# Performance work log

Hardware: AMD Instinct MI355X
Metric: run time of the kernel (lower is better)

Reference implementation:

```python
import jax, jax.numpy as jnp
import numpy as np

EMBED_DIM = 1024
NUM_HEADS = 16
HEAD_DIM = EMBED_DIM // NUM_HEADS
EPS = 1e-6


def setup_inputs() -> dict:
    key = jax.random.key(0)
    ks = jax.random.split(key, 10)
    B, S, D = 4, 2048, EMBED_DIM
    def xavier(k, shape):
        fan_in, fan_out = shape[1], shape[0]
        limit = float(np.sqrt(6.0 / (fan_in + fan_out)))
        return jax.random.uniform(k, shape, jnp.float32, -limit, limit)
    return {
        "x": jax.random.normal(ks[0], (B, S, D), jnp.float32),
        "ln_gamma": jnp.ones((D,), jnp.float32),
        "ln_beta": jnp.zeros((D,), jnp.float32),
        "Wq": xavier(ks[1], (D, D)), "bq": jnp.zeros((D,), jnp.float32),
        "Wk": xavier(ks[2], (D, D)), "bk": jnp.zeros((D,), jnp.float32),
        "Wv": xavier(ks[3], (D, D)), "bv": jnp.zeros((D,), jnp.float32),
        "Wo": xavier(ks[4], (D, D)), "bo": jnp.zeros((D,), jnp.float32),
    }


def reference(x, ln_gamma, ln_beta, Wq, bq, Wk, bk, Wv, bv, Wo, bo):
    B, S, D = x.shape
    # Pre-LayerNorm
    mu = jnp.mean(x, axis=-1, keepdims=True)
    var = jnp.mean((x - mu) ** 2, axis=-1, keepdims=True)
    xn = (x - mu) / jnp.sqrt(var + EPS) * ln_gamma + ln_beta
    # QKV projections (torch Linear: y = x @ W.T + b)
    def split_heads(t):  # [B,S,D] -> [B,H,S,hd]
        return t.reshape(B, S, NUM_HEADS, HEAD_DIM).transpose(0, 2, 1, 3)
    q = split_heads(xn @ Wq.T + bq)
    k = split_heads(xn @ Wk.T + bk)
    v = split_heads(xn @ Wv.T + bv)
    scale = 1.0 / jnp.sqrt(jnp.float32(HEAD_DIM))
    scores = jnp.einsum("bhqd,bhkd->bhqk", q, k) * scale
    probs = jax.nn.softmax(scores, axis=-1)  # dropout is identity (eval)
    ctx = jnp.einsum("bhqk,bhkd->bhqd", probs, v)
    ctx = ctx.transpose(0, 2, 1, 3).reshape(B, S, D)
    out = ctx @ Wo.T + bo  # proj dropout identity (eval)
    return out
```

## Files before the change

### kernel.cpp

```cpp
#include <hip/hip_runtime.h>
#include <hip/hip_bf16.h>
#include <stdint.h>

typedef __bf16 bf16x8 __attribute__((ext_vector_type(8)));
typedef float f32x4 __attribute__((ext_vector_type(4)));

#define LOG2E 1.44269504088896340736f

__device__ inline void gload_lds16(const void* g, void* l) {
  __builtin_amdgcn_global_load_lds((const __attribute__((address_space(1))) void*)g,
                                   (__attribute__((address_space(3))) void*)l, 16, 0, 0);
}

__device__ inline unsigned short bf16_bits(float f) {
  return __builtin_bit_cast(unsigned short, __float2bfloat16(f));
}

__device__ inline float fast_exp2(float x) {
  return __builtin_amdgcn_exp2f(x);
}

__device__ inline uint32_t cvtpk_bf16(float lo, float hi) {
  uint32_t d;
  asm("v_cvt_pk_bf16_f32 %0, %1, %2" : "=v"(d) : "v"(lo), "v"(hi));
  return d;
}
__device__ inline void plswap32(uint32_t& a, uint32_t& b) {
  asm("v_permlane32_swap_b32 %0, %1" : "+v"(a), "+v"(b));
}
__device__ inline void plswap16(uint32_t& a, uint32_t& b) {
  asm("v_permlane16_swap_b32 %0, %1" : "+v"(a), "+v"(b));
}

__global__ __launch_bounds__(256) void prep_kernel(
    const float* __restrict__ x, const float* __restrict__ gamma,
    const float* __restrict__ beta, __hip_bfloat16* __restrict__ xn,
    const float* __restrict__ Wq, const float* __restrict__ Wk,
    const float* __restrict__ Wv, const float* __restrict__ Wo,
    __hip_bfloat16* __restrict__ Wqk, __hip_bfloat16* __restrict__ Wvb,
    __hip_bfloat16* __restrict__ Wob)
{
  const int t = threadIdx.x;
  if (blockIdx.x < 8192) {
    const int row = blockIdx.x;
    const float4 v = reinterpret_cast<const float4*>(x + (size_t)row * 1024)[t];
    float s = v.x + v.y + v.z + v.w;
    float q = v.x*v.x + v.y*v.y + v.z*v.z + v.w*v.w;
    #pragma unroll
    for (int off = 32; off >= 1; off >>= 1) {
      s += __shfl_xor(s, off);
      q += __shfl_xor(q, off);
    }
    __shared__ float ls[4], lq[4];
    const int wave = t >> 6, lane = t & 63;
    if (lane == 0) { ls[wave] = s; lq[wave] = q; }
    __syncthreads();
    s = ls[0] + ls[1] + ls[2] + ls[3];
    q = lq[0] + lq[1] + lq[2] + lq[3];
    const float mean = s * (1.0f/1024.0f);
    const float var  = q * (1.0f/1024.0f) - mean*mean;
    const float rstd = rsqrtf(var + 1e-6f);
    const float4 gm = reinterpret_cast<const float4*>(gamma)[t];
    const float4 bt = reinterpret_cast<const float4*>(beta)[t];
    ushort4 o;
    o.x = bf16_bits((v.x - mean)*rstd*gm.x + bt.x);
    o.y = bf16_bits((v.y - mean)*rstd*gm.y + bt.y);
    o.z = bf16_bits((v.z - mean)*rstd*gm.z + bt.z);
    o.w = bf16_bits((v.w - mean)*rstd*gm.w + bt.w);
    reinterpret_cast<ushort4*>(xn + (size_t)row*1024)[t] = o;
  } else {
    const int cb = blockIdx.x - 8192;
    const int which = cb >> 10;
    const int i = (cb & 1023) * 256 + t;
    const float* src;
    __hip_bfloat16* dst;
    if (which == 0)      { src = Wq; dst = Wqk; }
    else if (which == 1) { src = Wk; dst = Wqk + 1024*1024; }
    else if (which == 2) { src = Wv; dst = Wvb; }
    else                 { src = Wo; dst = Wob; }
    const float4 v = reinterpret_cast<const float4*>(src)[i];
    ushort4 o;
    o.x = bf16_bits(v.x); o.y = bf16_bits(v.y);
    o.z = bf16_bits(v.z); o.w = bf16_bits(v.w);
    reinterpret_cast<ushort4*>(dst)[i] = o;
  }
}

__global__ __launch_bounds__(256) void qkv_gemm(
    const __hip_bfloat16* __restrict__ xn,
    const __hip_bfloat16* __restrict__ Wqk,
    const __hip_bfloat16* __restrict__ Wvb,
    const float* __restrict__ bq, const float* __restrict__ bk,
    const float* __restrict__ bv,
    __hip_bfloat16* __restrict__ Qb, __hip_bfloat16* __restrict__ Kb,
    __hip_bfloat16* __restrict__ Vt)
{
  constexpr int K = 1024;
  __shared__ __align__(16) __hip_bfloat16 Al[128*32];
  __shared__ __align__(16) __hip_bfloat16 Bl[128*32];
  const int t = threadIdx.x;
  const int wave = t >> 6, lane = t & 63;
  const int li = lane & 15, g = lane >> 4;
  const int wm = (wave >> 1) * 64, wn = (wave & 1) * 64;

  const int lin = blockIdx.x;
  const int wg  = (lin & 7) * 192 + (lin >> 3);
  const bool isV = wg >= 1024;
  int m0, n0;
  const __hip_bfloat16 *A, *B;
  if (!isV) {
    m0 = (wg >> 4) * 128; n0 = (wg & 15) * 128;
    A = xn; B = Wqk;
  } else {
    const int w2 = wg - 1024;
    m0 = (w2 & 7) * 128; n0 = (w2 >> 3) * 128;
    A = Wvb; B = xn;
  }
  const int srow = t >> 2, sch = (t & 3) * 8;

  const __hip_bfloat16* ga = A + (size_t)(m0 + srow) * K + sch;
  const __hip_bfloat16* gb = B + (size_t)(n0 + srow) * K + sch;

  f32x4 acc[4][4] = {};

  for (int kt = 0; kt < K; kt += 32) {
    gload_lds16(ga + kt,          Al + t*8);
    gload_lds16(ga + kt + 64*K,   Al + t*8 + 2048);
    gload_lds16(gb + kt,          Bl + t*8);
    gload_lds16(gb + kt + 64*K,   Bl + t*8 + 2048);
    __syncthreads();
    bf16x8 af[4], bfr[4];
    #pragma unroll
    for (int mi = 0; mi < 4; ++mi)
      af[mi] = *reinterpret_cast<const bf16x8*>(Al + (wm + mi*16 + li)*32 + g*8);
    #pragma unroll
    for (int ni = 0; ni < 4; ++ni)
      bfr[ni] = *reinterpret_cast<const bf16x8*>(Bl + (wn + ni*16 + li)*32 + g*8);
    #pragma unroll
    for (int mi = 0; mi < 4; ++mi)
      #pragma unroll
      for (int ni = 0; ni < 4; ++ni)
        acc[mi][ni] = __builtin_amdgcn_mfma_f32_16x16x32_bf16(af[mi], bfr[ni], acc[mi][ni], 0, 0, 0);
    __syncthreads();
  }

  #pragma unroll
  for (int mi = 0; mi < 4; ++mi) {
    #pragma unroll
    for (int ni = 0; ni < 4; ++ni) {
      #pragma unroll
      for (int r = 0; r < 4; ++r) {
        const int grow = m0 + wm + mi*16 + g*4 + r;
        const int gcol = n0 + wn + ni*16 + li;
        float v = acc[mi][ni][r];
        if (!isV) {
          const int b = grow >> 11, ss = grow & 2047;
          if (gcol < 1024) {
            v = (v + bq[gcol]) * (0.125f * LOG2E);
            const int h = gcol >> 6, d = gcol & 63;
            Qb[(((size_t)(b*16 + h))*2048 + ss)*64 + d] = __float2bfloat16(v);
          } else {
            const int c2 = gcol - 1024;
            v = v + bk[c2];
            const int h = c2 >> 6, d = c2 & 63;
            Kb[(((size_t)(b*16 + h))*2048 + ss)*64 + d] = __float2bfloat16(v);
          }
        } else {
          v += bv[grow];
          Vt[(size_t)grow*8192 + gcol] = __float2bfloat16(v);
        }
      }
    }
  }
}

__global__ __launch_bounds__(256) void out_gemm(
    const __hip_bfloat16* __restrict__ A,
    const __hip_bfloat16* __restrict__ B,
    const float* __restrict__ bias,
    float* __restrict__ C)
{
  constexpr int K = 1024;
  __shared__ __align__(16) __hip_bfloat16 Al[128*32];
  __shared__ __align__(16) __hip_bfloat16 Bl[128*32];
  const int t = threadIdx.x;
  const int wave = t >> 6, lane = t & 63;
  const int li = lane & 15, g = lane >> 4;
  const int wm = (wave >> 1) * 64, wn = (wave & 1) * 64;

  const int lin = blockIdx.y * gridDim.x + blockIdx.x;
  const int cpx = (gridDim.x * gridDim.y) >> 3;
  const int wg  = (lin & 7) * cpx + (lin >> 3);
  const int bx  = wg & (gridDim.x - 1);
  const int by  = wg >> __builtin_ctz(gridDim.x);
  const int m0 = by * 128, n0 = bx * 128;
  const int srow = t >> 2, sch = (t & 3) * 8;

  const __hip_bfloat16* ga = A + (size_t)(m0 + srow) * K + sch;
  const __hip_bfloat16* gb = B + (size_t)(n0 + srow) * K + sch;

  f32x4 acc[4][4] = {};

  for (int kt = 0; kt < K; kt += 32) {
    gload_lds16(ga + kt,          Al + t*8);
    gload_lds16(ga + kt + 64*K,   Al + t*8 + 2048);
    gload_lds16(gb + kt,          Bl + t*8);
    gload_lds16(gb + kt + 64*K,   Bl + t*8 + 2048);
    __syncthreads();
    bf16x8 af[4], bfr[4];
    #pragma unroll
    for (int mi = 0; mi < 4; ++mi)
      af[mi] = *reinterpret_cast<const bf16x8*>(Al + (wm + mi*16 + li)*32 + g*8);
    #pragma unroll
    for (int ni = 0; ni < 4; ++ni)
      bfr[ni] = *reinterpret_cast<const bf16x8*>(Bl + (wn + ni*16 + li)*32 + g*8);
    #pragma unroll
    for (int mi = 0; mi < 4; ++mi)
      #pragma unroll
      for (int ni = 0; ni < 4; ++ni)
        acc[mi][ni] = __builtin_amdgcn_mfma_f32_16x16x32_bf16(af[mi], bfr[ni], acc[mi][ni], 0, 0, 0);
    __syncthreads();
  }

  #pragma unroll
  for (int mi = 0; mi < 4; ++mi) {
    #pragma unroll
    for (int ni = 0; ni < 4; ++ni) {
      #pragma unroll
      for (int r = 0; r < 4; ++r) {
        const int grow = m0 + wm + mi*16 + g*4 + r;
        const int gcol = n0 + wn + ni*16 + li;
        C[(size_t)grow*1024 + gcol] = acc[mi][ni][r] + bias[gcol];
      }
    }
  }
}

__global__ __launch_bounds__(512, 8) void attn_kernel(
    const __hip_bfloat16* __restrict__ Q,
    const __hip_bfloat16* __restrict__ K,
    const __hip_bfloat16* __restrict__ Vt,
    __hip_bfloat16* __restrict__ ctx)
{
  const int t = threadIdx.x, wave = t >> 6, lane = t & 63;
  const int li = lane & 15, g = lane >> 4;

  const int lin = blockIdx.x;
  const int wg  = (lin & 7) * 128 + (lin >> 3);
  const int bh  = wg >> 4, qt = wg & 15;
  const int b = bh >> 4, h = bh & 15;
  const int qbase = qt * 128 + wave * 16;

  __shared__ __align__(16) __hip_bfloat16 Klds[2][4096];
  __shared__ __align__(16) __hip_bfloat16 Vlds[2][4096];

  const bf16x8* Qv = reinterpret_cast<const bf16x8*>(Q + ((size_t)bh*2048 + qbase + li)*64 + g*8);
  const bf16x8 aQ0 = Qv[0], aQ1 = Qv[4];

  f32x4 acc[4] = {};
  float l_par = 0.f;

  const __hip_bfloat16* Kbh = K + (size_t)bh*2048*64;
  const __hip_bfloat16* Vbh = Vt + (size_t)h*64*8192 + b*2048;

  const int row0 = t >> 3;
  const int scb_e = ((((t & 7) * 16) ^ ((row0 & 7) << 4)) >> 1);

  const int krd0 = (li*128 + ((g*16)      ^ ((li & 7) << 4))) >> 1;
  const int krd1 = (li*128 + ((g*16 + 64) ^ ((li & 7) << 4))) >> 1;

  gload_lds16(Kbh + (size_t)row0*64 + scb_e,        &Klds[0][t*8]);
  gload_lds16(Vbh + (size_t)row0*8192 + scb_e,      &Vlds[0][t*8]);
  gload_lds16(Kbh + (size_t)(64+row0)*64 + scb_e,   &Klds[1][t*8]);
  gload_lds16(Vbh + (size_t)row0*8192 + 64 + scb_e, &Vlds[1][t*8]);
  asm volatile("s_waitcnt vmcnt(2)" ::: "memory");
  __builtin_amdgcn_sched_barrier(0);
  __builtin_amdgcn_s_barrier();

  const __hip_bfloat16* kSrc = Kbh + (size_t)(128 + row0)*64 + scb_e;
  const __hip_bfloat16* vSrc = Vbh + (size_t)row0*8192 + 128 + scb_e;

  for (int it = 0; it < 32; ++it) {
    const int cur = it & 1;
    const __hip_bfloat16* Kc = Klds[cur];
    const __hip_bfloat16* Vc = Vlds[cur];

    f32x4 s[4] = {};
    __builtin_amdgcn_s_setprio(1);
    #pragma unroll
    for (int nt = 0; nt < 4; ++nt) {
      const bf16x8 k0 = *reinterpret_cast<const bf16x8*>(&Kc[nt*1024 + krd0]);
      const bf16x8 k1 = *reinterpret_cast<const bf16x8*>(&Kc[nt*1024 + krd1]);
      s[nt] = __builtin_amdgcn_mfma_f32_16x16x32_bf16(k0, aQ0, s[nt], 0, 0, 0);
      s[nt] = __builtin_amdgcn_mfma_f32_16x16x32_bf16(k1, aQ1, s[nt], 0, 0, 0);
    }
    __builtin_amdgcn_s_setprio(0);

    float sm = 0.f;
    #pragma unroll
    for (int nt = 0; nt < 4; ++nt)
      #pragma unroll
      for (int r = 0; r < 4; ++r) {
        const float p = fast_exp2(s[nt][r]); s[nt][r] = p; sm += p;
      }
    l_par += sm;

    union U8 { uint32_t w[4]; bf16x8 v; };
    bf16x8 aP0, aP1;
    {
      uint32_t c[4][2];
      #pragma unroll
      for (int nt = 0; nt < 4; ++nt) {
        c[nt][0] = cvtpk_bf16(s[nt][0], s[nt][1]);
        c[nt][1] = cvtpk_bf16(s[nt][2], s[nt][3]);
      }
      uint32_t x0 = c[0][0], y0 = c[1][0], x1 = c[0][1], y1 = c[1][1];
      plswap32(x0, y0); plswap32(x1, y1);
      plswap16(x0, y0); plswap16(x1, y1);
      U8 u0; u0.w[0] = x0; u0.w[1] = x1; u0.w[2] = y0; u0.w[3] = y1;
      aP0 = u0.v;
      uint32_t x2 = c[2][0], y2 = c[3][0], x3 = c[2][1], y3 = c[3][1];
      plswap32(x2, y2); plswap32(x3, y3);
      plswap16(x2, y2); plswap16(x3, y3);
      U8 u1; u1.w[0] = x2; u1.w[1] = x3; u1.w[2] = y2; u1.w[3] = y3;
      aP1 = u1.v;
    }

    __builtin_amdgcn_s_setprio(1);
    #pragma unroll
    for (int dt = 0; dt < 4; ++dt) {
      const bf16x8 v0 = *reinterpret_cast<const bf16x8*>(&Vc[dt*1024 + krd0]);
      const bf16x8 v1 = *reinterpret_cast<const bf16x8*>(&Vc[dt*1024 + krd1]);
      acc[dt] = __builtin_amdgcn_mfma_f32_16x16x32_bf16(v0, aP0, acc[dt], 0, 0, 0);
      acc[dt] = __builtin_amdgcn_mfma_f32_16x16x32_bf16(v1, aP1, acc[dt], 0, 0, 0);
    }
    __builtin_amdgcn_s_setprio(0);

    if (it < 31) {
      __builtin_amdgcn_s_barrier();
      if (it < 30) {
        gload_lds16(kSrc, &Klds[cur][t*8]);
        gload_lds16(vSrc, &Vlds[cur][t*8]);
        kSrc += 64*64;
        vSrc += 64;
        asm volatile("s_waitcnt vmcnt(2)" ::: "memory");
      } else {
        asm volatile("s_waitcnt vmcnt(0)" ::: "memory");
      }
      __builtin_amdgcn_sched_barrier(0);
      __builtin_amdgcn_s_barrier();
    }
  }

  l_par += __shfl_xor(l_par, 16);
  l_par += __shfl_xor(l_par, 32);
  const float inv = 1.0f / l_par;

  __hip_bfloat16* cp = ctx + ((size_t)(b*2048 + qbase))*1024 + h*64;
  #pragma unroll
  for (int dt = 0; dt < 4; ++dt) {
    ushort4 o;
    o.x = bf16_bits(acc[dt][0] * inv);
    o.y = bf16_bits(acc[dt][1] * inv);
    o.z = bf16_bits(acc[dt][2] * inv);
    o.w = bf16_bits(acc[dt][3] * inv);
    *reinterpret_cast<ushort4*>(&cp[(size_t)li*1024 + dt*16 + g*4]) = o;
  }
}

extern "C" void kernel_launch(void* const* d_in, const int* in_sizes, int n_in,
                              void* d_out, int out_size, void* d_ws, size_t ws_size,
                              hipStream_t stream)
{
  const float* x  = (const float*)d_in[0];
  const float* g  = (const float*)d_in[1];
  const float* be = (const float*)d_in[2];
  const float* Wq = (const float*)d_in[3];
  const float* bq = (const float*)d_in[4];
  const float* Wk = (const float*)d_in[5];
  const float* bk = (const float*)d_in[6];
  const float* Wv = (const float*)d_in[7];
  const float* bv = (const float*)d_in[8];
  const float* Wo = (const float*)d_in[9];
  const float* bo = (const float*)d_in[10];
  float* out = (float*)d_out;

  char* ws = (char*)d_ws;
  __hip_bfloat16* xn  = (__hip_bfloat16*)(ws);
  __hip_bfloat16* Wqk = (__hip_bfloat16*)(ws + 16777216);
  __hip_bfloat16* Wvb = (__hip_bfloat16*)(ws + 20971520);
  __hip_bfloat16* Wob = (__hip_bfloat16*)(ws + 23068672);
  __hip_bfloat16* Qb  = (__hip_bfloat16*)(ws + 25165824);
  __hip_bfloat16* Kb  = (__hip_bfloat16*)(ws + 41943040);
  __hip_bfloat16* Vt  = (__hip_bfloat16*)(ws + 58720256);
  __hip_bfloat16* ctx = (__hip_bfloat16*)(ws + 75497472);

  prep_kernel<<<12288, 256, 0, stream>>>(x, g, be, xn, Wq, Wk, Wv, Wo, Wqk, Wvb, Wob);
  qkv_gemm<<<1536, 256, 0, stream>>>(xn, Wqk, Wvb, bq, bk, bv, Qb, Kb, Vt);
  attn_kernel<<<1024, 512, 0, stream>>>(Qb, Kb, Vt, ctx);
  out_gemm<<<dim3(8, 64), 256, 0, stream>>>(ctx, Wob, bo, out);
}
```

Baseline: 203.4 us.

## Share one GEMM body with K-tile 64, XOR-swizzled LDS and MFMA priority

Both projection GEMMs now use a shared templated body that loads 64-wide K tiles (half as many barrier pairs) into an XOR-swizzled LDS layout, which is meant to avoid bank conflicts on the fragment reads. s_setprio is raised around the MFMA block so the scheduler favours the math waves. LDS per block doubles, which can lower occupancy. The out_gemm grid also becomes 1D with its own tile remapping.

```diff
diff --git a/kernel.cpp b/kernel.cpp
--- a/kernel.cpp
+++ b/kernel.cpp
@@ -86,6 +86,99 @@
   }
 }
 
+template<int MODE>
+__device__ __forceinline__ void gemm_body(
+    const __hip_bfloat16* __restrict__ A,
+    const __hip_bfloat16* __restrict__ B,
+    int m0, int n0,
+    const float* __restrict__ bias0,
+    const float* __restrict__ bias1,
+    void* __restrict__ C0,
+    void* __restrict__ C1,
+    __hip_bfloat16* Al, __hip_bfloat16* Bl)
+{
+  constexpr int K = 1024;
+  const int t = threadIdx.x;
+  const int wave = t >> 6, lane = t & 63;
+  const int li = lane & 15, g = lane >> 4;
+  const int wm = (wave >> 1) * 64, wn = (wave & 1) * 64;
+
+  const int srow = t >> 3;
+  const int scb_e = ((((t & 7) * 16) ^ ((srow & 7) << 4)) >> 1);
+  const __hip_bfloat16* ga = A + (size_t)(m0 + srow) * K + scb_e;
+  const __hip_bfloat16* gb = B + (size_t)(n0 + srow) * K + scb_e;
+
+  const int swz = (li & 7) << 4;
+  const int rdk[2] = { ((0*64 + 0) ^ 0), 0 };
+  (void)rdk;
+  const int rd0 = (((g*16)      ^ swz) >> 1);
+  const int rd1 = (((g*16 + 64) ^ swz) >> 1);
+
+  f32x4 acc[4][4] = {};
+
+  for (int kt = 0; kt < K; kt += 64) {
+    #pragma unroll
+    for (int i = 0; i < 4; ++i) {
+      gload_lds16(ga + (size_t)(i*32)*K + kt, Al + i*2048 + t*8);
+      gload_lds16(gb + (size_t)(i*32)*K + kt, Bl + i*2048 + t*8);
+    }
+    __syncthreads();
+    bf16x8 af[4][2], bfr[4][2];
+    #pragma unroll
+    for (int mi = 0; mi < 4; ++mi) {
+      af[mi][0] = *reinterpret_cast<const bf16x8*>(&Al[(wm + mi*16 + li)*64 + rd0]);
+      af[mi][1] = *reinterpret_cast<const bf16x8*>(&Al[(wm + mi*16 + li)*64 + rd1]);
+    }
+    #pragma unroll
+    for (int ni = 0; ni < 4; ++ni) {
+      bfr[ni][0] = *reinterpret_cast<const bf16x8*>(&Bl[(wn + ni*16 + li)*64 + rd0]);
+      bfr[ni][1] = *reinterpret_cast<const bf16x8*>(&Bl[(wn + ni*16 + li)*64 + rd1]);
+    }
+    __builtin_amdgcn_s_setprio(1);
+    #pragma unroll
+    for (int mi = 0; mi < 4; ++mi)
+      #pragma unroll
+      for (int ni = 0; ni < 4; ++ni) {
+        acc[mi][ni] = __builtin_amdgcn_mfma_f32_16x16x32_bf16(af[mi][0], bfr[ni][0], acc[mi][ni], 0, 0, 0);
+        acc[mi][ni] = __builtin_amdgcn_mfma_f32_16x16x32_bf16(af[mi][1], bfr[ni][1], acc[mi][ni], 0, 0, 0);
+      }
+    __builtin_amdgcn_s_setprio(0);
+    __syncthreads();
+  }
+
+  #pragma unroll
+  for (int mi = 0; mi < 4; ++mi) {
+    #pragma unroll
+    for (int ni = 0; ni < 4; ++ni) {
+      #pragma unroll
+      for (int r = 0; r < 4; ++r) {
+        const int grow = m0 + wm + mi*16 + g*4 + r;
+        const int gcol = n0 + wn + ni*16 + li;
+        float v = acc[mi][ni][r];
+        if constexpr (MODE == 0) {
+          const int b = grow >> 11, ss = grow & 2047;
+          if (gcol < 1024) {
+            v = (v + bias0[gcol]) * (0.125f * LOG2E);
+            const int h = gcol >> 6, d = gcol & 63;
+            ((__hip_bfloat16*)C0)[(((size_t)(b*16 + h))*2048 + ss)*64 + d] = __float2bfloat16(v);
+          } else {
+            const int c2 = gcol - 1024;
+            v = v + bias1[c2];
+            const int h = c2 >> 6, d = c2 & 63;
+            ((__hip_bfloat16*)C1)[(((size_t)(b*16 + h))*2048 + ss)*64 + d] = __float2bfloat16(v);
+          }
+        } else if constexpr (MODE == 1) {
+          v += bias0[grow];
+          ((__hip_bfloat16*)C0)[(size_t)grow*8192 + gcol] = __float2bfloat16(v);
+        } else {
+          v += bias0[gcol];
+          ((float*)C0)[(size_t)grow*1024 + gcol] = v;
+        }
+      }
+    }
+  }
+}
+
 __global__ __launch_bounds__(256) void qkv_gemm(
     const __hip_bfloat16* __restrict__ xn,
     const __hip_bfloat16* __restrict__ Wqk,
@@ -95,82 +188,17 @@
     __hip_bfloat16* __restrict__ Qb, __hip_bfloat16* __restrict__ Kb,
     __hip_bfloat16* __restrict__ Vt)
 {
-  constexpr int K = 1024;
-  __shared__ __align__(16) __hip_bfloat16 Al[128*32];
-  __shared__ __align__(16) __hip_bfloat16 Bl[128*32];
-  const int t = threadIdx.x;
-  const int wave = t >> 6, lane = t & 63;
-  const int li = lane & 15, g = lane >> 4;
-  const int wm = (wave >> 1) * 64, wn = (wave & 1) * 64;
-
+  __shared__ __align__(16) __hip_bfloat16 Al[128*64];
+  __shared__ __align__(16) __hip_bfloat16 Bl[128*64];
   const int lin = blockIdx.x;
   const int wg  = (lin & 7) * 192 + (lin >> 3);
-  const bool isV = wg >= 1024;
-  int m0, n0;
-  const __hip_bfloat16 *A, *B;
-  if (!isV) {
-    m0 = (wg >> 4) * 128; n0 = (wg & 15) * 128;
-    A = xn; B = Wqk;
+  if (wg < 1024) {
+    const int m0 = (wg >> 4) * 128, n0 = (wg & 15) * 128;
+    gemm_body<0>(xn, Wqk, m0, n0, bq, bk, Qb, Kb, Al, Bl);
   } else {
     const int w2 = wg - 1024;
-    m0 = (w2 & 7) * 128; n0 = (w2 >> 3) * 128;
-    A = Wvb; B = xn;
-  }
-  const int srow = t >> 2, sch = (t & 3) * 8;
-
-  const __hip_bfloat16* ga = A + (size_t)(m0 + srow) * K + sch;
-  const __hip_bfloat16* gb = B + (size_t)(n0 + srow) * K + sch;
-
-  f32x4 acc[4][4] = {};
-
-  for (int kt = 0; kt < K; kt += 32) {
-    gload_lds16(ga + kt,          Al + t*8);
-    gload_lds16(ga + kt + 64*K,   Al + t*8 + 2048);
-    gload_lds16(gb + kt,          Bl + t*8);
-    gload_lds16(gb + kt + 64*K,   Bl + t*8 + 2048);
-    __syncthreads();
-    bf16x8 af[4], bfr[4];
-    #pragma unroll
-    for (int mi = 0; mi < 4; ++mi)
-      af[mi] = *reinterpret_cast<const bf16x8*>(Al + (wm + mi*16 + li)*32 + g*8);
-    #pragma unroll
-    for (int ni = 0; ni < 4; ++ni)
-      bfr[ni] = *reinterpret_cast<const bf16x8*>(Bl + (wn + ni*16 + li)*32 + g*8);
-    #pragma unroll
-    for (int mi = 0; mi < 4; ++mi)
-      #pragma unroll
-      for (int ni = 0; ni < 4; ++ni)
-        acc[mi][ni] = __builtin_amdgcn_mfma_f32_16x16x32_bf16(af[mi], bfr[ni], acc[mi][ni], 0, 0, 0);
-    __syncthreads();
-  }
-
-  #pragma unroll
-  for (int mi = 0; mi < 4; ++mi) {
-    #pragma unroll
-    for (int ni = 0; ni < 4; ++ni) {
-      #pragma unroll
-      for (int r = 0; r < 4; ++r) {
-        const int grow = m0 + wm + mi*16 + g*4 + r;
-        const int gcol = n0 + wn + ni*16 + li;
-        float v = acc[mi][ni][r];
-        if (!isV) {
-          const int b = grow >> 11, ss = grow & 2047;
-          if (gcol < 1024) {
-            v = (v + bq[gcol]) * (0.125f * LOG2E);
-            const int h = gcol >> 6, d = gcol & 63;
-            Qb[(((size_t)(b*16 + h))*2048 + ss)*64 + d] = __float2bfloat16(v);
-          } else {
-            const int c2 = gcol - 1024;
-            v = v + bk[c2];
-            const int h = c2 >> 6, d = c2 & 63;
-            Kb[(((size_t)(b*16 + h))*2048 + ss)*64 + d] = __float2bfloat16(v);
-          }
-        } else {
-          v += bv[grow];
-          Vt[(size_t)grow*8192 + gcol] = __float2bfloat16(v);
-        }
-      }
-    }
+    const int m0 = (w2 & 7) * 128, n0 = (w2 >> 3) * 128;
+    gemm_body<1>(Wvb, xn, m0, n0, bv, nullptr, Vt, nullptr, Al, Bl);
   }
 }
 
@@ -180,60 +208,12 @@
     const float* __restrict__ bias,
     float* __restrict__ C)
 {
-  constexpr int K = 1024;
-  __shared__ __align__(16) __hip_bfloat16 Al[128*32];
-  __shared__ __align__(16) __hip_bfloat16 Bl[128*32];
-  const int t = threadIdx.x;
-  const int wave = t >> 6, lane = t & 63;
-  const int li = lane & 15, g = lane >> 4;
-  const int wm = (wave >> 1) * 64, wn = (wave & 1) * 64;
-
-  const int lin = blockIdx.y * gridDim.x + blockIdx.x;
-  const int cpx = (gridDim.x * gridDim.y) >> 3;
-  const int wg  = (lin & 7) * cpx + (lin >> 3);
-  const int bx  = wg & (gridDim.x - 1);
-  const int by  = wg >> __builtin_ctz(gridDim.x);
-  const int m0 = by * 128, n0 = bx * 128;
-  const int srow = t >> 2, sch = (t & 3) * 8;
-
-  const __hip_bfloat16* ga = A + (size_t)(m0 + srow) * K + sch;
-  const __hip_bfloat16* gb = B + (size_t)(n0 + srow) * K + sch;
-
-  f32x4 acc[4][4] = {};
-
-  for (int kt = 0; kt < K; kt += 32) {
-    gload_lds16(ga + kt,          Al + t*8);
-    gload_lds16(ga + kt + 64*K,   Al + t*8 + 2048);
-    gload_lds16(gb + kt,          Bl + t*8);
-    gload_lds16(gb + kt + 64*K,   Bl + t*8 + 2048);
-    __syncthreads();
-    bf16x8 af[4], bfr[4];
-    #pragma unroll
-    for (int mi = 0; mi < 4; ++mi)
-      af[mi] = *reinterpret_cast<const bf16x8*>(Al + (wm + mi*16 + li)*32 + g*8);
-    #pragma unroll
-    for (int ni = 0; ni < 4; ++ni)
-      bfr[ni] = *reinterpret_cast<const bf16x8*>(Bl + (wn + ni*16 + li)*32 + g*8);
-    #pragma unroll
-    for (int mi = 0; mi < 4; ++mi)
-      #pragma unroll
-      for (int ni = 0; ni < 4; ++ni)
-        acc[mi][ni] = __builtin_amdgcn_mfma_f32_16x16x32_bf16(af[mi], bfr[ni], acc[mi][ni], 0, 0, 0);
-    __syncthreads();
-  }
-
-  #pragma unroll
-  for (int mi = 0; mi < 4; ++mi) {
-    #pragma unroll
-    for (int ni = 0; ni < 4; ++ni) {
-      #pragma unroll
-      for (int r = 0; r < 4; ++r) {
-        const int grow = m0 + wm + mi*16 + g*4 + r;
-        const int gcol = n0 + wn + ni*16 + li;
-        C[(size_t)grow*1024 + gcol] = acc[mi][ni][r] + bias[gcol];
-      }
-    }
-  }
+  __shared__ __align__(16) __hip_bfloat16 Al[128*64];
+  __shared__ __align__(16) __hip_bfloat16 Bl[128*64];
+  const int lin = blockIdx.x;
+  const int wg  = (lin & 7) * 64 + (lin >> 3);
+  const int m0 = (wg >> 3) * 128, n0 = (wg & 7) * 128;
+  gemm_body<2>(A, B, m0, n0, bias, nullptr, C, nullptr, Al, Bl);
 }
 
 __global__ __launch_bounds__(512, 8) void attn_kernel(
@@ -398,5 +378,5 @@
   prep_kernel<<<12288, 256, 0, stream>>>(x, g, be, xn, Wq, Wk, Wv, Wo, Wqk, Wvb, Wob);
   qkv_gemm<<<1536, 256, 0, stream>>>(xn, Wqk, Wvb, bq, bk, bv, Qb, Kb, Vt);
   attn_kernel<<<1024, 512, 0, stream>>>(Qb, Kb, Vt, ctx);
-  out_gemm<<<dim3(8, 64), 256, 0, stream>>>(ctx, Wob, bo, out);
-}
+  out_gemm<<<512, 256, 0, stream>>>(ctx, Wob, bo, out);
+}
```

Result: faster. 194.0 us (-4.6%).
